# Performance work log

Measured on AMD Instinct MI355X. Metric: run time of the kernel, lower is better.

Reference implementation:

```python
import jax, jax.numpy as jnp
import numpy as np

EPS = 1e-5

def _bn(x, gamma, beta):
    # training-mode BatchNorm1d over (batch, points) per channel; x: [B, C, N]
    mean = x.mean(axis=(0, 2), keepdims=True)
    var = x.var(axis=(0, 2), keepdims=True)
    return gamma[None, :, None] * (x - mean) * jax.lax.rsqrt(var + EPS) + beta[None, :, None]

def _conv_nn(x, idx, W, b):
    # x: [B, Cin, N_in]; idx: [N_out, k]; W: [Cout, Cin, k]
    g = x[:, :, idx]  # gather -> [B, Cin, N_out, k]
    return jnp.einsum('bink,oik->bon', g, W) + b[None, :, None]

def setup_inputs() -> dict:
    key = jax.random.key(0)
    ks = jax.random.split(key, 8)
    B, Cin, Cout = 32, 32, 64
    Nin, Nout, K, KP = 32768, 8192, 9, 4
    s = 0.05
    return {
        'x': jax.random.normal(ks[0], (B, Cin, Nin), jnp.float32),
        'W1': jax.random.normal(ks[1], (Cout, Cin, K), jnp.float32) * s,
        'b1': jnp.zeros((Cout,), jnp.float32),
        'W2': jax.random.normal(ks[2], (Cout, Cout, K), jnp.float32) * s,
        'b2': jnp.zeros((Cout,), jnp.float32),
        'We': jax.random.normal(ks[3], (Cout, Cin), jnp.float32) * s,
        'be': jnp.zeros((Cout,), jnp.float32),
        'g1': jnp.ones((Cout,), jnp.float32), 'beta1': jnp.zeros((Cout,), jnp.float32),
        'g2': jnp.ones((Cout,), jnp.float32), 'beta2': jnp.zeros((Cout,), jnp.float32),
        'g3': jnp.ones((Cout,), jnp.float32), 'beta3': jnp.zeros((Cout,), jnp.float32),
        'idx1': jax.random.randint(ks[4], (Nout, K), 0, Nin, jnp.int32),
        'idx2': jax.random.randint(ks[5], (Nout, K), 0, Nout, jnp.int32),
        'pool_idx': jax.random.randint(ks[6], (Nout, KP), 0, Nin, jnp.int32),
    }

def reference(x, W1, b1, W2, b2, We, be, g1, beta1, g2, beta2, g3, beta3, idx1, idx2, pool_idx):
    # main branch: ConvNN -> BN -> ReLU -> ConvNN -> BN
    out = jax.nn.relu(_bn(_conv_nn(x, idx1, W1, b1), g1, beta1))
    out = _bn(_conv_nn(out, idx2, W2, b2), g2, beta2)
    # shortcut: AvgPoolNN (k=4) -> 1x1 conv expand -> BN
    pooled = x[:, :, pool_idx].mean(axis=-1)  # [B, Cin, N_out]
    identity = _bn(jnp.einsum('bin,oi->bon', pooled, We) + be[None, :, None], g3, beta3)
    return jax.nn.relu(out + identity)
```

## Files before the change

kernel.cpp:

```cpp
#include <hip/hip_runtime.h>
#include <hip/hip_bf16.h>

typedef __attribute__((ext_vector_type(8))) short short8_t;
typedef __attribute__((ext_vector_type(4))) float f32x4_t;

#define NOUT 8192
#define NIN 32768
#define MTOT 262144.0f
#define ST_STRIPES 64

#define MF(a,b,c) __builtin_amdgcn_mfma_f32_16x16x32_bf16((a),(b),(c),0,0,0)

static __device__ __forceinline__ float bf2f(ushort u) {
    union { float f; unsigned int i; } x; x.i = ((unsigned int)u) << 16; return x.f;
}
static __device__ __forceinline__ ushort f2bfx(float f) {
    union { __hip_bfloat16 h; ushort u; } v;
    v.h = __float2bfloat16(f);
    return v.u;
}
static __device__ __forceinline__ short8_t i4s8(int4 v) {
    union { int4 i; short8_t s; } u; u.i = v; return u.s;
}

static __device__ __forceinline__ short8_t bn8(int4 v, const float* a8, const float* c8) {
    ushort* pv = (ushort*)&v;
    #pragma unroll
    for (int e = 0; e < 8; ++e)
        pv[e] = f2bfx(fmaxf(a8[e] * bf2f(pv[e]) + c8[e], 0.f));
    return i4s8(v);
}

__global__ __launch_bounds__(256) void transpose_x_kernel(
    const float* __restrict__ x, ushort* __restrict__ xt)
{
    __shared__ ushort T[64][66];
    const int tid = threadIdx.x;
    const int n0 = blockIdx.x * 64, c0 = blockIdx.y * 64;
    const int lane64 = tid & 63, rb = (tid >> 6) * 16;
    #pragma unroll
    for (int r = 0; r < 16; ++r) {
        int c_l = rb + r;
        T[c_l][lane64] = f2bfx(x[(size_t)(c0 + c_l) * NIN + n0 + lane64]);
    }
    __syncthreads();
    #pragma unroll
    for (int r = 0; r < 16; ++r) {
        int n_l = rb + r;
        xt[(size_t)(n0 + n_l) * 1024 + c0 + lane64] = T[lane64][n_l];
    }
}

__global__ __launch_bounds__(256) void prep_w_kernel(
    const float* __restrict__ W1, const float* __restrict__ W2,
    const float* __restrict__ We,
    ushort* __restrict__ w1p, ushort* __restrict__ w2p, ushort* __restrict__ wep,
    float* __restrict__ stz)
{
    int t = blockIdx.x * 256 + threadIdx.x;
    const int N1 = 18432, N2 = 36864, N3 = 2048;
    if (t < 3 * ST_STRIPES * 128) stz[t] = 0.f;
    if (t < N1) {
        int e = t & 7, o = (t >> 3) & 63, seg = t >> 9;
        int fcg = seg & 3, k = seg >> 2;
        int i = fcg * 8 + e;
        w1p[t] = f2bfx(W1[o * 288 + i * 9 + k]);
    } else if (t < N1 + N2) {
        int t2 = t - N1;
        int e = t2 & 7, o = (t2 >> 3) & 63, seg = t2 >> 9;
        int fcg = seg & 3, kk = (seg >> 2) & 1, k = seg >> 3;
        int ci = kk * 32 + fcg * 8 + e;
        w2p[t2] = f2bfx(W2[o * 576 + ci * 9 + k]);
    } else if (t < N1 + N2 + N3) {
        int t3 = t - N1 - N2;
        wep[t3] = f2bfx(We[t3]);
    }
}

__global__ __launch_bounds__(512, 4) void conv1_kernel(
    const ushort* __restrict__ xt, const int* __restrict__ idx1,
    const ushort* __restrict__ w1p, ushort* __restrict__ out1,
    float* __restrict__ st)
{
    __shared__ __align__(16) ushort Wl[18432];
    __shared__ float Ls[128];
    const int tid = threadIdx.x;
    const int lane = tid & 63, wv = tid >> 6;
    const int n = __builtin_amdgcn_readfirstlane(blockIdx.x * 8 + wv);
    const int l15 = lane & 15, fcg = lane >> 4, fc = fcg * 8;

    for (int i = tid; i < 2304; i += 512)
        ((int4*)Wl)[i] = ((const int4*)w1p)[i];
    if (tid < 128) Ls[tid] = 0.f;

    int rows[9];
    {
        const int* idxn = idx1 + n * 9;
        #pragma unroll
        for (int t = 0; t < 9; ++t) rows[t] = idxn[t];
    }
    __syncthreads();

    f32x4_t acc[2][4];
    #pragma unroll
    for (int m = 0; m < 2; ++m)
        #pragma unroll
        for (int nt = 0; nt < 4; ++nt) acc[m][nt] = (f32x4_t){0.f, 0.f, 0.f, 0.f};

    int4 A0[2], A1[2], A2[2], A3[2];

#define C1_PRE(K, A) { \
    const ushort* rp = xt + (size_t)rows[K] * 1024 + l15 * 32 + fc; \
    A[0] = *(const int4*)rp;           \
    A[1] = *(const int4*)(rp + 512);   }

#define C1_BODY(K, A) { \
    const ushort* wp = Wl + ((K) * 4 + fcg) * 512; \
    short8_t b0 = *(const short8_t*)(wp + l15 * 8); \
    short8_t b1 = *(const short8_t*)(wp + (16 + l15) * 8); \
    short8_t b2 = *(const short8_t*)(wp + (32 + l15) * 8); \
    short8_t b3 = *(const short8_t*)(wp + (48 + l15) * 8); \
    short8_t af0 = i4s8(A[0]), af1 = i4s8(A[1]); \
    acc[0][0] = MF(af0, b0, acc[0][0]); acc[1][0] = MF(af1, b0, acc[1][0]); \
    acc[0][1] = MF(af0, b1, acc[0][1]); acc[1][1] = MF(af1, b1, acc[1][1]); \
    acc[0][2] = MF(af0, b2, acc[0][2]); acc[1][2] = MF(af1, b2, acc[1][2]); \
    acc[0][3] = MF(af0, b3, acc[0][3]); acc[1][3] = MF(af1, b3, acc[1][3]); }

    C1_PRE(0, A0); C1_PRE(1, A1); C1_PRE(2, A2); C1_PRE(3, A3);
    C1_BODY(0, A0); C1_PRE(4, A0);
    C1_BODY(1, A1); C1_PRE(5, A1);
    C1_BODY(2, A2); C1_PRE(6, A2);
    C1_BODY(3, A3); C1_PRE(7, A3);
    C1_BODY(4, A0); C1_PRE(8, A0);
    C1_BODY(5, A1);
    C1_BODY(6, A2);
    C1_BODY(7, A3);
    C1_BODY(8, A0);
#undef C1_PRE
#undef C1_BODY

    const size_t outbase = (size_t)n * 2048;
    #pragma unroll
    for (int m = 0; m < 2; ++m)
        #pragma unroll
        for (int nt = 0; nt < 4; ++nt)
            #pragma unroll
            for (int j = 0; j < 4; ++j) {
                int b = m * 16 + (lane >> 4) * 4 + j;
                int o = nt * 16 + l15;
                out1[outbase + b * 64 + o] = f2bfx(acc[m][nt][j]);
            }
    #pragma unroll
    for (int nt = 0; nt < 4; ++nt) {
        float s = 0.f, q = 0.f;
        #pragma unroll
        for (int m = 0; m < 2; ++m)
            #pragma unroll
            for (int j = 0; j < 4; ++j) { float v = acc[m][nt][j]; s += v; q += v * v; }
        s += __shfl_xor(s, 16); s += __shfl_xor(s, 32);
        q += __shfl_xor(q, 16); q += __shfl_xor(q, 32);
        if (lane < 16) {
            atomicAdd(&Ls[nt * 16 + lane], s);
            atomicAdd(&Ls[64 + nt * 16 + lane], q);
        }
    }
    __syncthreads();
    if (tid < 128) atomicAdd(&st[(blockIdx.x & (ST_STRIPES - 1)) * 128 + tid], Ls[tid]);
}

__global__ __launch_bounds__(512, 4) void conv2_kernel(
    const ushort* __restrict__ out1raw, const int* __restrict__ idx2,
    const ushort* __restrict__ w2p, const float* __restrict__ ac1,
    ushort* __restrict__ out2, float* __restrict__ st)
{
    __shared__ __align__(16) ushort Wl[36864];
    __shared__ float Ls[128];
    const int tid = threadIdx.x;
    const int lane = tid & 63, wv = tid >> 6;
    const int n = __builtin_amdgcn_readfirstlane(blockIdx.x * 8 + wv);
    const int l15 = lane & 15, fcg = lane >> 4, fc = fcg * 8;

    for (int i = tid; i < 4608; i += 512)
        ((int4*)Wl)[i] = ((const int4*)w2p)[i];
    if (tid < 128) Ls[tid] = 0.f;

    int rows[9];
    {
        const int* idxn = idx2 + n * 9;
        #pragma unroll
        for (int t = 0; t < 9; ++t) rows[t] = idxn[t];
    }
    float a0r[8], c0r[8], a1r[8], c1r[8];
    #pragma unroll
    for (int e = 0; e < 8; ++e) {
        a0r[e] = ac1[fc + e];       c0r[e] = ac1[64 + fc + e];
        a1r[e] = ac1[32 + fc + e];  c1r[e] = ac1[96 + fc + e];
    }
    __syncthreads();

    f32x4_t acc[2][4];
    #pragma unroll
    for (int m = 0; m < 2; ++m)
        #pragma unroll
        for (int nt = 0; nt < 4; ++nt) acc[m][nt] = (f32x4_t){0.f, 0.f, 0.f, 0.f};

    int4 A0[4], A1[4], A2[4];

#define C2_PRE(K, A) { \
    const ushort* rp = out1raw + (size_t)rows[K] * 2048 + l15 * 64 + fc; \
    A[0] = *(const int4*)rp;           \
    A[1] = *(const int4*)(rp + 32);    \
    A[2] = *(const int4*)(rp + 1024);  \
    A[3] = *(const int4*)(rp + 1056);  }

#define C2_BODY(K, A) { \
    const ushort* wp0 = Wl + ((K) * 8 + fcg) * 512;         \
    const ushort* wp1 = wp0 + 4 * 512;                       \
    short8_t b00 = *(const short8_t*)(wp0 + l15 * 8); \
    short8_t b10 = *(const short8_t*)(wp0 + (16 + l15) * 8); \
    short8_t b20 = *(const short8_t*)(wp0 + (32 + l15) * 8); \
    short8_t b30 = *(const short8_t*)(wp0 + (48 + l15) * 8); \
    short8_t b01 = *(const short8_t*)(wp1 + l15 * 8); \
    short8_t b11 = *(const short8_t*)(wp1 + (16 + l15) * 8); \
    short8_t b21 = *(const short8_t*)(wp1 + (32 + l15) * 8); \
    short8_t b31 = *(const short8_t*)(wp1 + (48 + l15) * 8); \
    short8_t af00 = bn8(A[0], a0r, c0r); \
    short8_t af01 = bn8(A[1], a1r, c1r); \
    short8_t af10 = bn8(A[2], a0r, c0r); \
    short8_t af11 = bn8(A[3], a1r, c1r); \
    acc[0][0] = MF(af00, b00, acc[0][0]); acc[0][0] = MF(af01, b01, acc[0][0]); \
    acc[0][1] = MF(af00, b10, acc[0][1]); acc[0][1] = MF(af01, b11, acc[0][1]); \
    acc[0][2] = MF(af00, b20, acc[0][2]); acc[0][2] = MF(af01, b21, acc[0][2]); \
    acc[0][3] = MF(af00, b30, acc[0][3]); acc[0][3] = MF(af01, b31, acc[0][3]); \
    acc[1][0] = MF(af10, b00, acc[1][0]); acc[1][0] = MF(af11, b01, acc[1][0]); \
    acc[1][1] = MF(af10, b10, acc[1][1]); acc[1][1] = MF(af11, b11, acc[1][1]); \
    acc[1][2] = MF(af10, b20, acc[1][2]); acc[1][2] = MF(af11, b21, acc[1][2]); \
    acc[1][3] = MF(af10, b30, acc[1][3]); acc[1][3] = MF(af11, b31, acc[1][3]); }

    C2_PRE(0, A0); C2_PRE(1, A1); C2_PRE(2, A2);
    C2_BODY(0, A0); C2_PRE(3, A0);
    C2_BODY(1, A1); C2_PRE(4, A1);
    C2_BODY(2, A2); C2_PRE(5, A2);
    C2_BODY(3, A0); C2_PRE(6, A0);
    C2_BODY(4, A1); C2_PRE(7, A1);
    C2_BODY(5, A2); C2_PRE(8, A2);
    C2_BODY(6, A0);
    C2_BODY(7, A1);
    C2_BODY(8, A2);
#undef C2_PRE
#undef C2_BODY

    const size_t outbase = (size_t)n * 2048;
    #pragma unroll
    for (int m = 0; m < 2; ++m)
        #pragma unroll
        for (int nt = 0; nt < 4; ++nt)
            #pragma unroll
            for (int j = 0; j < 4; ++j) {
                int b = m * 16 + (lane >> 4) * 4 + j;
                int o = nt * 16 + l15;
                out2[outbase + b * 64 + o] = f2bfx(acc[m][nt][j]);
            }
    #pragma unroll
    for (int nt = 0; nt < 4; ++nt) {
        float s = 0.f, q = 0.f;
        #pragma unroll
        for (int m = 0; m < 2; ++m)
            #pragma unroll
            for (int j = 0; j < 4; ++j) { float v = acc[m][nt][j]; s += v; q += v * v; }
        s += __shfl_xor(s, 16); s += __shfl_xor(s, 32);
        q += __shfl_xor(q, 16); q += __shfl_xor(q, 32);
        if (lane < 16) {
            atomicAdd(&Ls[nt * 16 + lane], s);
            atomicAdd(&Ls[64 + nt * 16 + lane], q);
        }
    }
    __syncthreads();
    if (tid < 128) atomicAdd(&st[(blockIdx.x & (ST_STRIPES - 1)) * 128 + tid], Ls[tid]);
}

__global__ __launch_bounds__(256) void ident_kernel(
    const ushort* __restrict__ xt, const int* __restrict__ pool_idx,
    const ushort* __restrict__ wep, ushort* __restrict__ identt,
    float* __restrict__ st)
{
    __shared__ float Ls[128];
    const int tid = threadIdx.x;
    const int lane = tid & 63, wv = tid >> 6;
    const int n = __builtin_amdgcn_readfirstlane(blockIdx.x * 4 + wv);
    const int l15 = lane & 15, fc = (lane >> 4) * 8;

    const ushort* wpf = wep + l15 * 32 + fc;
    short8_t bfr[4];
    #pragma unroll
    for (int nt = 0; nt < 4; ++nt)
        bfr[nt] = *(const short8_t*)(wpf + nt * 512);

    int prow[4];
    {
        const int* pn = pool_idx + n * 4;
        #pragma unroll
        for (int t = 0; t < 4; ++t) prow[t] = pn[t];
    }
    if (tid < 128) Ls[tid] = 0.f;

    float s0[8], s1[8];
    #pragma unroll
    for (int e = 0; e < 8; ++e) { s0[e] = 0.f; s1[e] = 0.f; }
    #pragma unroll
    for (int kp = 0; kp < 4; ++kp) {
        const ushort* rp = xt + (size_t)prow[kp] * 1024 + l15 * 32 + fc;
        int4 v0 = *(const int4*)rp;
        int4 v1 = *(const int4*)(rp + 512);
        const ushort* p0 = (const ushort*)&v0;
        const ushort* p1 = (const ushort*)&v1;
        #pragma unroll
        for (int e = 0; e < 8; ++e) { s0[e] += bf2f(p0[e]); s1[e] += bf2f(p1[e]); }
    }
    short8_t af0, af1;
    {
        int4 v0, v1; ushort* p0 = (ushort*)&v0; ushort* p1 = (ushort*)&v1;
        #pragma unroll
        for (int e = 0; e < 8; ++e) {
            p0[e] = f2bfx(s0[e] * 0.25f);
            p1[e] = f2bfx(s1[e] * 0.25f);
        }
        af0 = i4s8(v0); af1 = i4s8(v1);
    }

    f32x4_t acc[2][4];
    #pragma unroll
    for (int nt = 0; nt < 4; ++nt) {
        acc[0][nt] = (f32x4_t){0.f, 0.f, 0.f, 0.f};
        acc[1][nt] = (f32x4_t){0.f, 0.f, 0.f, 0.f};
        acc[0][nt] = MF(af0, bfr[nt], acc[0][nt]);
        acc[1][nt] = MF(af1, bfr[nt], acc[1][nt]);
    }

    const size_t outbase = (size_t)n * 2048;
    #pragma unroll
    for (int m = 0; m < 2; ++m)
        #pragma unroll
        for (int nt = 0; nt < 4; ++nt)
            #pragma unroll
            for (int j = 0; j < 4; ++j) {
                int b = m * 16 + (lane >> 4) * 4 + j;
                int o = nt * 16 + l15;
                identt[outbase + b * 64 + o] = f2bfx(acc[m][nt][j]);
            }
    #pragma unroll
    for (int nt = 0; nt < 4; ++nt) {
        float s = 0.f, q = 0.f;
        #pragma unroll
        for (int m = 0; m < 2; ++m)
            #pragma unroll
            for (int j = 0; j < 4; ++j) { float v = acc[m][nt][j]; s += v; q += v * v; }
        s += __shfl_xor(s, 16); s += __shfl_xor(s, 32);
        q += __shfl_xor(q, 16); q += __shfl_xor(q, 32);
        if (lane < 16) {
            atomicAdd(&Ls[nt * 16 + lane], s);
            atomicAdd(&Ls[64 + nt * 16 + lane], q);
        }
    }
    __syncthreads();
    if (tid < 128) atomicAdd(&st[(blockIdx.x & (ST_STRIPES - 1)) * 128 + tid], Ls[tid]);
}

__global__ void finalize_kernel(const float* __restrict__ st, const float* __restrict__ g,
                                const float* __restrict__ bet, float* __restrict__ ac)
{
    int o = threadIdx.x;
    if (o >= 64) return;
    float s = 0.f, q = 0.f;
    for (int i = 0; i < ST_STRIPES; ++i) { s += st[i * 128 + o]; q += st[i * 128 + 64 + o]; }
    float mean = s * (1.0f / MTOT);
    float var  = q * (1.0f / MTOT) - mean * mean;
    float a = g[o] * rsqrtf(var + 1e-5f);
    ac[o] = a;
    ac[64 + o] = bet[o] - a * mean;
}

__global__ void finalize23_kernel(
    const float* __restrict__ st2, const float* __restrict__ g2, const float* __restrict__ b2,
    const float* __restrict__ st3, const float* __restrict__ g3, const float* __restrict__ b3,
    float* __restrict__ ac2, float* __restrict__ ac3)
{
    int o = threadIdx.x;
    if (o >= 64) return;
    const float* st = blockIdx.x ? st3 : st2;
    const float* g  = blockIdx.x ? g3  : g2;
    const float* bt = blockIdx.x ? b3  : b2;
    float* ac       = blockIdx.x ? ac3 : ac2;
    float s = 0.f, q = 0.f;
    for (int i = 0; i < ST_STRIPES; ++i) { s += st[i * 128 + o]; q += st[i * 128 + 64 + o]; }
    float mean = s * (1.0f / MTOT);
    float var  = q * (1.0f / MTOT) - mean * mean;
    float a = g[o] * rsqrtf(var + 1e-5f);
    ac[o] = a;
    ac[64 + o] = bt[o] - a * mean;
}

__global__ __launch_bounds__(256) void final_combine_kernel(
    const ushort* __restrict__ out2, const ushort* __restrict__ idt,
    const float* __restrict__ ac2, const float* __restrict__ ac3,
    float* __restrict__ dout)
{
    __shared__ float tile[64][65];
    const int tid = threadIdx.x;
    const int n0 = blockIdx.x * 64, bo0 = blockIdx.y * 64;
    const int lane64 = tid & 63, rb = (tid >> 6) * 16;
    const int o = lane64;
    const float a2 = ac2[o], c2 = ac2[64 + o], a3 = ac3[o], c3 = ac3[64 + o];
    #pragma unroll
    for (int r = 0; r < 16; ++r) {
        int n_l = rb + r;
        size_t p = (size_t)(n0 + n_l) * 2048 + bo0 + lane64;
        float v = a2 * bf2f(out2[p]) + c2 + a3 * bf2f(idt[p]) + c3;
        tile[n_l][lane64] = fmaxf(v, 0.f);
    }
    __syncthreads();
    #pragma unroll
    for (int r = 0; r < 16; ++r) {
        int bo_l = rb + r;
        dout[(size_t)(bo0 + bo_l) * NOUT + n0 + lane64] = tile[lane64][bo_l];
    }
}

extern "C" void kernel_launch(void* const* d_in, const int* in_sizes, int n_in,
                              void* d_out, int out_size, void* d_ws, size_t ws_size,
                              hipStream_t stream)
{
    const float* x     = (const float*)d_in[0];
    const float* W1    = (const float*)d_in[1];
    const float* W2    = (const float*)d_in[3];
    const float* We    = (const float*)d_in[5];
    const float* g1    = (const float*)d_in[7];
    const float* beta1 = (const float*)d_in[8];
    const float* g2    = (const float*)d_in[9];
    const float* beta2 = (const float*)d_in[10];
    const float* g3    = (const float*)d_in[11];
    const float* beta3 = (const float*)d_in[12];
    const int* idx1    = (const int*)d_in[13];
    const int* idx2    = (const int*)d_in[14];
    const int* pool_idx= (const int*)d_in[15];
    float* dout = (float*)d_out;

    char* ws = (char*)d_ws;
    const size_t off_xt   = 0;
    const size_t off_out1 = 67108864;
    const size_t off_out2 = 100663296;
    const size_t off_id   = 134217728;
    const size_t off_w1p  = 167772160;
    const size_t off_w2p  = 167809024;
    const size_t off_wep  = 167882752;
    const size_t off_st   = 167886848;
    const size_t off_ac   = 167985152;
    const size_t need     = 167986688;
    if (ws_size < need) return;

    ushort* xt   = (ushort*)(ws + off_xt);
    ushort* out1 = (ushort*)(ws + off_out1);
    ushort* out2 = (ushort*)(ws + off_out2);
    ushort* idt  = (ushort*)(ws + off_id);
    ushort* w1p  = (ushort*)(ws + off_w1p);
    ushort* w2p  = (ushort*)(ws + off_w2p);
    ushort* wep  = (ushort*)(ws + off_wep);
    float*  st1  = (float*)(ws + off_st);
    float*  st2  = st1 + 64 * 128;
    float*  st3  = st1 + 2 * 64 * 128;
    float*  ac1  = (float*)(ws + off_ac);
    float*  ac2  = ac1 + 128;
    float*  ac3  = ac1 + 256;

    prep_w_kernel<<<224, 256, 0, stream>>>(W1, W2, We, w1p, w2p, wep, st1);
    transpose_x_kernel<<<dim3(512, 16), 256, 0, stream>>>(x, xt);
    conv1_kernel<<<1024, 512, 0, stream>>>(xt, idx1, w1p, out1, st1);
    ident_kernel<<<2048, 256, 0, stream>>>(xt, pool_idx, wep, idt, st3);
    finalize_kernel<<<1, 64, 0, stream>>>(st1, g1, beta1, ac1);
    conv2_kernel<<<1024, 512, 0, stream>>>(out1, idx2, w2p, ac1, out2, st2);
    finalize23_kernel<<<2, 64, 0, stream>>>(st2, g2, beta2, st3, g3, beta3, ac2, ac3);
    final_combine_kernel<<<dim3(128, 32), 256, 0, stream>>>(out2, idt, ac2, ac3, dout);
}
```

Baseline: 180.1 us.

## Fuse shortcut pooling branch into conv1 kernel and enlarge blocks to 1024 threads

The avgpool+1x1 expand shortcut is merged into the conv1 kernel. Its gathers are issued in the freed register slots of the conv1 prefetch pipeline, and its BN stats are accumulated alongside conv1's. Both conv kernels move to 1024-thread blocks (16 points per block), and sched_barriers are inserted to pin the load/MFMA interleave. The goal is to drop one kernel launch, halve per-block weight staging into LDS, and overlap the pooling loads with conv1 compute. The costs are higher register pressure and a different occupancy profile.

```diff
diff --git a/kernel.cpp b/kernel.cpp
--- a/kernel.cpp
+++ b/kernel.cpp
@@ -8,6 +8,7 @@
 #define NIN 32768
 #define MTOT 262144.0f
 #define ST_STRIPES 64
+#define SB() __builtin_amdgcn_sched_barrier(0)
 
 #define MF(a,b,c) __builtin_amdgcn_mfma_f32_16x16x32_bf16((a),(b),(c),0,0,0)
 
@@ -77,27 +78,32 @@
     }
 }
 
-__global__ __launch_bounds__(512, 4) void conv1_kernel(
+__global__ __launch_bounds__(1024, 2) void conv1i_kernel(
     const ushort* __restrict__ xt, const int* __restrict__ idx1,
-    const ushort* __restrict__ w1p, ushort* __restrict__ out1,
-    float* __restrict__ st)
+    const int* __restrict__ pool_idx, const ushort* __restrict__ w1p,
+    const ushort* __restrict__ wep,
+    ushort* __restrict__ out1, ushort* __restrict__ identt,
+    float* __restrict__ st1g, float* __restrict__ st3g)
 {
     __shared__ __align__(16) ushort Wl[18432];
-    __shared__ float Ls[128];
+    __shared__ float Ls1[128], Ls3[128];
     const int tid = threadIdx.x;
     const int lane = tid & 63, wv = tid >> 6;
-    const int n = __builtin_amdgcn_readfirstlane(blockIdx.x * 8 + wv);
+    const int n = __builtin_amdgcn_readfirstlane(blockIdx.x * 16 + wv);
     const int l15 = lane & 15, fcg = lane >> 4, fc = fcg * 8;
 
-    for (int i = tid; i < 2304; i += 512)
+    for (int i = tid; i < 2304; i += 1024)
         ((int4*)Wl)[i] = ((const int4*)w1p)[i];
-    if (tid < 128) Ls[tid] = 0.f;
-
-    int rows[9];
+    if (tid < 128) { Ls1[tid] = 0.f; Ls3[tid] = 0.f; }
+
+    int rows[9], prow[4];
     {
         const int* idxn = idx1 + n * 9;
         #pragma unroll
         for (int t = 0; t < 9; ++t) rows[t] = idxn[t];
+        const int* pn = pool_idx + n * 4;
+        #pragma unroll
+        for (int t = 0; t < 4; ++t) prow[t] = pn[t];
     }
     __syncthreads();
 
@@ -111,8 +117,13 @@
 
 #define C1_PRE(K, A) { \
     const ushort* rp = xt + (size_t)rows[K] * 1024 + l15 * 32 + fc; \
-    A[0] = *(const int4*)rp;           \
-    A[1] = *(const int4*)(rp + 512);   }
+    A[0] = *(const int4*)rp; \
+    A[1] = *(const int4*)(rp + 512); }
+
+#define C1_PPRE(KP, A) { \
+    const ushort* rp = xt + (size_t)prow[KP] * 1024 + l15 * 32 + fc; \
+    A[0] = *(const int4*)rp; \
+    A[1] = *(const int4*)(rp + 512); }
 
 #define C1_BODY(K, A) { \
     const ushort* wp = Wl + ((K) * 4 + fcg) * 512; \
@@ -126,15 +137,15 @@
     acc[0][2] = MF(af0, b2, acc[0][2]); acc[1][2] = MF(af1, b2, acc[1][2]); \
     acc[0][3] = MF(af0, b3, acc[0][3]); acc[1][3] = MF(af1, b3, acc[1][3]); }
 
-    C1_PRE(0, A0); C1_PRE(1, A1); C1_PRE(2, A2); C1_PRE(3, A3);
-    C1_BODY(0, A0); C1_PRE(4, A0);
-    C1_BODY(1, A1); C1_PRE(5, A1);
-    C1_BODY(2, A2); C1_PRE(6, A2);
-    C1_BODY(3, A3); C1_PRE(7, A3);
-    C1_BODY(4, A0); C1_PRE(8, A0);
-    C1_BODY(5, A1);
-    C1_BODY(6, A2);
-    C1_BODY(7, A3);
+    C1_PRE(0, A0); C1_PRE(1, A1); C1_PRE(2, A2); C1_PRE(3, A3); SB();
+    C1_BODY(0, A0); C1_PRE(4, A0); SB();
+    C1_BODY(1, A1); C1_PRE(5, A1); SB();
+    C1_BODY(2, A2); C1_PRE(6, A2); SB();
+    C1_BODY(3, A3); C1_PRE(7, A3); SB();
+    C1_BODY(4, A0); C1_PRE(8, A0); SB();
+    C1_BODY(5, A1); C1_PPRE(0, A1); SB();
+    C1_BODY(6, A2); C1_PPRE(1, A2); SB();
+    C1_BODY(7, A3); C1_PPRE(2, A3); SB();
     C1_BODY(8, A0);
 #undef C1_PRE
 #undef C1_BODY
@@ -160,15 +171,83 @@
         s += __shfl_xor(s, 16); s += __shfl_xor(s, 32);
         q += __shfl_xor(q, 16); q += __shfl_xor(q, 32);
         if (lane < 16) {
-            atomicAdd(&Ls[nt * 16 + lane], s);
-            atomicAdd(&Ls[64 + nt * 16 + lane], q);
+            atomicAdd(&Ls1[nt * 16 + lane], s);
+            atomicAdd(&Ls1[64 + nt * 16 + lane], q);
         }
     }
-    __syncthreads();
-    if (tid < 128) atomicAdd(&st[(blockIdx.x & (ST_STRIPES - 1)) * 128 + tid], Ls[tid]);
-}
-
-__global__ __launch_bounds__(512, 4) void conv2_kernel(
+
+    int4 P3[2];
+    C1_PPRE(3, P3);
+#undef C1_PPRE
+    float s0[8], s1[8];
+    #pragma unroll
+    for (int e = 0; e < 8; ++e) { s0[e] = 0.f; s1[e] = 0.f; }
+    {
+        const int4* bufs[4][2] = {{&A1[0],&A1[1]},{&A2[0],&A2[1]},{&A3[0],&A3[1]},{&P3[0],&P3[1]}};
+        #pragma unroll
+        for (int kp = 0; kp < 4; ++kp) {
+            const ushort* p0 = (const ushort*)bufs[kp][0];
+            const ushort* p1 = (const ushort*)bufs[kp][1];
+            #pragma unroll
+            for (int e = 0; e < 8; ++e) { s0[e] += bf2f(p0[e]); s1[e] += bf2f(p1[e]); }
+        }
+    }
+    short8_t paf0, paf1;
+    {
+        int4 v0, v1; ushort* p0 = (ushort*)&v0; ushort* p1 = (ushort*)&v1;
+        #pragma unroll
+        for (int e = 0; e < 8; ++e) {
+            p0[e] = f2bfx(s0[e] * 0.25f);
+            p1[e] = f2bfx(s1[e] * 0.25f);
+        }
+        paf0 = i4s8(v0); paf1 = i4s8(v1);
+    }
+    short8_t bfr[4];
+    {
+        const ushort* wpf = wep + l15 * 32 + fc;
+        #pragma unroll
+        for (int nt = 0; nt < 4; ++nt)
+            bfr[nt] = *(const short8_t*)(wpf + nt * 512);
+    }
+    #pragma unroll
+    for (int nt = 0; nt < 4; ++nt) {
+        acc[0][nt] = (f32x4_t){0.f, 0.f, 0.f, 0.f};
+        acc[1][nt] = (f32x4_t){0.f, 0.f, 0.f, 0.f};
+        acc[0][nt] = MF(paf0, bfr[nt], acc[0][nt]);
+        acc[1][nt] = MF(paf1, bfr[nt], acc[1][nt]);
+    }
+    #pragma unroll
+    for (int m = 0; m < 2; ++m)
+        #pragma unroll
+        for (int nt = 0; nt < 4; ++nt)
+            #pragma unroll
+            for (int j = 0; j < 4; ++j) {
+                int b = m * 16 + (lane >> 4) * 4 + j;
+                int o = nt * 16 + l15;
+                identt[outbase + b * 64 + o] = f2bfx(acc[m][nt][j]);
+            }
+    #pragma unroll
+    for (int nt = 0; nt < 4; ++nt) {
+        float s = 0.f, q = 0.f;
+        #pragma unroll
+        for (int m = 0; m < 2; ++m)
+            #pragma unroll
+            for (int j = 0; j < 4; ++j) { float v = acc[m][nt][j]; s += v; q += v * v; }
+        s += __shfl_xor(s, 16); s += __shfl_xor(s, 32);
+        q += __shfl_xor(q, 16); q += __shfl_xor(q, 32);
+        if (lane < 16) {
+            atomicAdd(&Ls3[nt * 16 + lane], s);
+            atomicAdd(&Ls3[64 + nt * 16 + lane], q);
+        }
+    }
+    __syncthreads();
+    if (tid < 128) {
+        atomicAdd(&st1g[(blockIdx.x & (ST_STRIPES - 1)) * 128 + tid], Ls1[tid]);
+        atomicAdd(&st3g[(blockIdx.x & (ST_STRIPES - 1)) * 128 + tid], Ls3[tid]);
+    }
+}
+
+__global__ __launch_bounds__(1024, 2) void conv2_kernel(
     const ushort* __restrict__ out1raw, const int* __restrict__ idx2,
     const ushort* __restrict__ w2p, const float* __restrict__ ac1,
     ushort* __restrict__ out2, float* __restrict__ st)
@@ -177,10 +256,10 @@
     __shared__ float Ls[128];
     const int tid = threadIdx.x;
     const int lane = tid & 63, wv = tid >> 6;
-    const int n = __builtin_amdgcn_readfirstlane(blockIdx.x * 8 + wv);
+    const int n = __builtin_amdgcn_readfirstlane(blockIdx.x * 16 + wv);
     const int l15 = lane & 15, fcg = lane >> 4, fc = fcg * 8;
 
-    for (int i = tid; i < 4608; i += 512)
+    for (int i = tid; i < 4608; i += 1024)
         ((int4*)Wl)[i] = ((const int4*)w2p)[i];
     if (tid < 128) Ls[tid] = 0.f;
 
@@ -208,14 +287,14 @@
 
 #define C2_PRE(K, A) { \
     const ushort* rp = out1raw + (size_t)rows[K] * 2048 + l15 * 64 + fc; \
-    A[0] = *(const int4*)rp;           \
-    A[1] = *(const int4*)(rp + 32);    \
-    A[2] = *(const int4*)(rp + 1024);  \
-    A[3] = *(const int4*)(rp + 1056);  }
+    A[0] = *(const int4*)rp; \
+    A[1] = *(const int4*)(rp + 32); \
+    A[2] = *(const int4*)(rp + 1024); \
+    A[3] = *(const int4*)(rp + 1056); }
 
 #define C2_BODY(K, A) { \
-    const ushort* wp0 = Wl + ((K) * 8 + fcg) * 512;         \
-    const ushort* wp1 = wp0 + 4 * 512;                       \
+    const ushort* wp0 = Wl + ((K) * 8 + fcg) * 512; \
+    const ushort* wp1 = wp0 + 4 * 512; \
     short8_t b00 = *(const short8_t*)(wp0 + l15 * 8); \
     short8_t b10 = *(const short8_t*)(wp0 + (16 + l15) * 8); \
     short8_t b20 = *(const short8_t*)(wp0 + (32 + l15) * 8); \
@@ -237,13 +316,13 @@
     acc[1][2] = MF(af10, b20, acc[1][2]); acc[1][2] = MF(af11, b21, acc[1][2]); \
     acc[1][3] = MF(af10, b30, acc[1][3]); acc[1][3] = MF(af11, b31, acc[1][3]); }
 
-    C2_PRE(0, A0); C2_PRE(1, A1); C2_PRE(2, A2);
-    C2_BODY(0, A0); C2_PRE(3, A0);
-    C2_BODY(1, A1); C2_PRE(4, A1);
-    C2_BODY(2, A2); C2_PRE(5, A2);
-    C2_BODY(3, A0); C2_PRE(6, A0);
-    C2_BODY(4, A1); C2_PRE(7, A1);
-    C2_BODY(5, A2); C2_PRE(8, A2);
+    C2_PRE(0, A0); C2_PRE(1, A1); C2_PRE(2, A2); SB();
+    C2_BODY(0, A0); C2_PRE(3, A0); SB();
+    C2_BODY(1, A1); C2_PRE(4, A1); SB();
+    C2_BODY(2, A2); C2_PRE(5, A2); SB();
+    C2_BODY(3, A0); C2_PRE(6, A0); SB();
+    C2_BODY(4, A1); C2_PRE(7, A1); SB();
+    C2_BODY(5, A2); C2_PRE(8, A2); SB();
     C2_BODY(6, A0);
     C2_BODY(7, A1);
     C2_BODY(8, A2);
@@ -260,93 +339,6 @@
                 int b = m * 16 + (lane >> 4) * 4 + j;
                 int o = nt * 16 + l15;
                 out2[outbase + b * 64 + o] = f2bfx(acc[m][nt][j]);
-            }
-    #pragma unroll
-    for (int nt = 0; nt < 4; ++nt) {
-        float s = 0.f, q = 0.f;
-        #pragma unroll
-        for (int m = 0; m < 2; ++m)
-            #pragma unroll
-            for (int j = 0; j < 4; ++j) { float v = acc[m][nt][j]; s += v; q += v * v; }
-        s += __shfl_xor(s, 16); s += __shfl_xor(s, 32);
-        q += __shfl_xor(q, 16); q += __shfl_xor(q, 32);
-        if (lane < 16) {
-            atomicAdd(&Ls[nt * 16 + lane], s);
-            atomicAdd(&Ls[64 + nt * 16 + lane], q);
-        }
-    }
-    __syncthreads();
-    if (tid < 128) atomicAdd(&st[(blockIdx.x & (ST_STRIPES - 1)) * 128 + tid], Ls[tid]);
-}
-
-__global__ __launch_bounds__(256) void ident_kernel(
-    const ushort* __restrict__ xt, const int* __restrict__ pool_idx,
-    const ushort* __restrict__ wep, ushort* __restrict__ identt,
-    float* __restrict__ st)
-{
-    __shared__ float Ls[128];
-    const int tid = threadIdx.x;
-    const int lane = tid & 63, wv = tid >> 6;
-    const int n = __builtin_amdgcn_readfirstlane(blockIdx.x * 4 + wv);
-    const int l15 = lane & 15, fc = (lane >> 4) * 8;
-
-    const ushort* wpf = wep + l15 * 32 + fc;
-    short8_t bfr[4];
-    #pragma unroll
-    for (int nt = 0; nt < 4; ++nt)
-        bfr[nt] = *(const short8_t*)(wpf + nt * 512);
-
-    int prow[4];
-    {
-        const int* pn = pool_idx + n * 4;
-        #pragma unroll
-        for (int t = 0; t < 4; ++t) prow[t] = pn[t];
-    }
-    if (tid < 128) Ls[tid] = 0.f;
-
-    float s0[8], s1[8];
-    #pragma unroll
-    for (int e = 0; e < 8; ++e) { s0[e] = 0.f; s1[e] = 0.f; }
-    #pragma unroll
-    for (int kp = 0; kp < 4; ++kp) {
-        const ushort* rp = xt + (size_t)prow[kp] * 1024 + l15 * 32 + fc;
-        int4 v0 = *(const int4*)rp;
-        int4 v1 = *(const int4*)(rp + 512);
-        const ushort* p0 = (const ushort*)&v0;
-        const ushort* p1 = (const ushort*)&v1;
-        #pragma unroll
-        for (int e = 0; e < 8; ++e) { s0[e] += bf2f(p0[e]); s1[e] += bf2f(p1[e]); }
-    }
-    short8_t af0, af1;
-    {
-        int4 v0, v1; ushort* p0 = (ushort*)&v0; ushort* p1 = (ushort*)&v1;
-        #pragma unroll
-        for (int e = 0; e < 8; ++e) {
-            p0[e] = f2bfx(s0[e] * 0.25f);
-            p1[e] = f2bfx(s1[e] * 0.25f);
-        }
-        af0 = i4s8(v0); af1 = i4s8(v1);
-    }
-
-    f32x4_t acc[2][4];
-    #pragma unroll
-    for (int nt = 0; nt < 4; ++nt) {
-        acc[0][nt] = (f32x4_t){0.f, 0.f, 0.f, 0.f};
-        acc[1][nt] = (f32x4_t){0.f, 0.f, 0.f, 0.f};
-        acc[0][nt] = MF(af0, bfr[nt], acc[0][nt]);
-        acc[1][nt] = MF(af1, bfr[nt], acc[1][nt]);
-    }
-
-    const size_t outbase = (size_t)n * 2048;
-    #pragma unroll
-    for (int m = 0; m < 2; ++m)
-        #pragma unroll
-        for (int nt = 0; nt < 4; ++nt)
-            #pragma unroll
-            for (int j = 0; j < 4; ++j) {
-                int b = m * 16 + (lane >> 4) * 4 + j;
-                int o = nt * 16 + l15;
-                identt[outbase + b * 64 + o] = f2bfx(acc[m][nt][j]);
             }
     #pragma unroll
     for (int nt = 0; nt < 4; ++nt) {
@@ -380,17 +372,17 @@
     ac[64 + o] = bet[o] - a * mean;
 }
 
-__global__ void finalize23_kernel(
-    const float* __restrict__ st2, const float* __restrict__ g2, const float* __restrict__ b2,
-    const float* __restrict__ st3, const float* __restrict__ g3, const float* __restrict__ b3,
-    float* __restrict__ ac2, float* __restrict__ ac3)
+__global__ void finalize_dual_kernel(
+    const float* __restrict__ stA, const float* __restrict__ gA, const float* __restrict__ bA,
+    const float* __restrict__ stB, const float* __restrict__ gB, const float* __restrict__ bB,
+    float* __restrict__ acA, float* __restrict__ acB)
 {
     int o = threadIdx.x;
     if (o >= 64) return;
-    const float* st = blockIdx.x ? st3 : st2;
-    const float* g  = blockIdx.x ? g3  : g2;
-    const float* bt = blockIdx.x ? b3  : b2;
-    float* ac       = blockIdx.x ? ac3 : ac2;
+    const float* st = blockIdx.x ? stB : stA;
+    const float* g  = blockIdx.x ? gB  : gA;
+    const float* bt = blockIdx.x ? bB  : bA;
+    float* ac       = blockIdx.x ? acB : acA;
     float s = 0.f, q = 0.f;
     for (int i = 0; i < ST_STRIPES; ++i) { s += st[i * 128 + o]; q += st[i * 128 + 64 + o]; }
     float mean = s * (1.0f / MTOT);
@@ -474,10 +466,9 @@
 
     prep_w_kernel<<<224, 256, 0, stream>>>(W1, W2, We, w1p, w2p, wep, st1);
     transpose_x_kernel<<<dim3(512, 16), 256, 0, stream>>>(x, xt);
-    conv1_kernel<<<1024, 512, 0, stream>>>(xt, idx1, w1p, out1, st1);
-    ident_kernel<<<2048, 256, 0, stream>>>(xt, pool_idx, wep, idt, st3);
-    finalize_kernel<<<1, 64, 0, stream>>>(st1, g1, beta1, ac1);
-    conv2_kernel<<<1024, 512, 0, stream>>>(out1, idx2, w2p, ac1, out2, st2);
-    finalize23_kernel<<<2, 64, 0, stream>>>(st2, g2, beta2, st3, g3, beta3, ac2, ac3);
+    conv1i_kernel<<<512, 1024, 0, stream>>>(xt, idx1, pool_idx, w1p, wep, out1, idt, st1, st3);
+    finalize_dual_kernel<<<2, 64, 0, stream>>>(st1, g1, beta1, st3, g3, beta3, ac1, ac3);
+    conv2_kernel<<<512, 1024, 0, stream>>>(out1, idx2, w2p, ac1, out2, st2);
+    finalize_kernel<<<1, 64, 0, stream>>>(st2, g2, beta2, ac2);
     final_combine_kernel<<<dim3(128, 32), 256, 0, stream>>>(out2, idt, ac2, ac3, dout);
 }
```

Measured after the change: 304.5 us. +69.1%, slower.
